# Kernel tuning notes

Measured on AMD Instinct MI355X. Metric: run time of the kernel, lower is better.

## Reference

```python
import jax, jax.numpy as jnp
import numpy as np

B, T, D, H = 4, 2048, 1024, 16
HD = D // H  # 64
LOCAL_CTX, BLOCKSIZE, VERTSIZE = 256, 1, 16
STRIDE = LOCAL_CTX // BLOCKSIZE  # 256


def build_fixed_mask(n):
    # num_verts == 1 branch of generate_fixed_attention_mask
    layout = np.zeros((n, n), dtype=np.bool_)
    # vertical stripes: top `vertsize` indices of each stride block
    for idx in range(STRIDE - VERTSIZE, STRIDE):
        layout[:, idx::STRIDE] = True
    rows = np.arange(n)
    # local: each query attends to its own stride-block
    same_block = (rows[:, None] // STRIDE) == (rows[None, :] // STRIDE)
    layout |= same_block
    # causal: zero out k > q
    layout &= rows[None, :] <= rows[:, None]
    return layout


def setup_inputs() -> dict:
    key = jax.random.key(0)
    k1, k2, k3, k4, k5 = jax.random.split(key, 5)
    s = 0.02
    return {
        "x": jax.random.normal(k1, (B, T, D), dtype=jnp.float32),
        "Wqkv": jax.random.normal(k2, (D, 3 * D), dtype=jnp.float32) * s,
        "bqkv": jax.random.normal(k3, (3 * D,), dtype=jnp.float32) * s,
        "Wproj": jax.random.normal(k4, (D, D), dtype=jnp.float32) * s,
        "bproj": jax.random.normal(k5, (D,), dtype=jnp.float32) * s,
        "mask": jnp.asarray(build_fixed_mask(T)),
    }


def reference(x, Wqkv, bqkv, Wproj, bproj, mask):
    b, t, _ = x.shape
    qkv = (x @ Wqkv + bqkv).reshape(b, t, 3, H, HD)
    # (B,T,3,H,HD) -> (B,H,T,HD) per component
    q = qkv[:, :, 0].transpose(0, 2, 1, 3)
    k = qkv[:, :, 1].transpose(0, 2, 1, 3)
    v = qkv[:, :, 2].transpose(0, 2, 1, 3)
    att = jnp.einsum("bhqd,bhkd->bhqk", q, k) * (1.0 / jnp.sqrt(jnp.float32(HD)))
    att = jnp.where(mask[:t, :t], att, -jnp.inf)
    att = jax.nn.softmax(att, axis=-1)
    y = jnp.einsum("bhqk,bhkd->bhqd", att, v)
    y = y.transpose(0, 2, 1, 3).reshape(b, t, D)
    return y @ Wproj + bproj
```

## Files before the change

kernel.cpp:

```cpp
#include <hip/hip_runtime.h>
#include <cstdint>
#include <cstddef>

typedef unsigned short u16;
typedef __attribute__((ext_vector_type(8))) short short8;
typedef __attribute__((ext_vector_type(4))) float f32x4;
typedef __attribute__((ext_vector_type(4))) unsigned short u16x4;

#define B_ 4
#define T_ 2048
#define D_ 1024
#define H_ 16
#define HD_ 64

__device__ __forceinline__ u16 f2bf(float f) {
  union { float f; unsigned i; } v; v.f = f;
  unsigned r = (v.i + 0x7FFFu + ((v.i >> 16) & 1u)) >> 16;
  return (u16)r;
}

__device__ __forceinline__ void load_lds16(const void* g, void* l) {
  __builtin_amdgcn_global_load_lds(
      (const __attribute__((address_space(1))) void*)g,
      (__attribute__((address_space(3))) void*)l, 16, 0, 0);
}

__global__ __launch_bounds__(256) void cvt_f32_bf16(const float* __restrict__ src,
                                                    u16* __restrict__ dst) {
  const size_t i = ((size_t)blockIdx.x * 256 + threadIdx.x) * 4;
  const f32x4 v = *(const f32x4*)(src + i);
  u16x4 o;
#pragma unroll
  for (int r = 0; r < 4; ++r) o[r] = f2bf(v[r]);
  *(u16x4*)(dst + i) = o;
}

__global__ __launch_bounds__(256) void transpose_cvt(const float* __restrict__ src,
                                                     u16* __restrict__ dst,
                                                     int R, int C) {
  __shared__ u16 t[32][33];
  const int c0 = blockIdx.x * 32, r0 = blockIdx.y * 32;
  const int tid = threadIdx.x;
  const int lr = tid >> 5, lc = tid & 31;
#pragma unroll
  for (int p = 0; p < 4; ++p)
    t[lr + p * 8][lc] = f2bf(src[(size_t)(r0 + lr + p * 8) * C + c0 + lc]);
  __syncthreads();
#pragma unroll
  for (int p = 0; p < 4; ++p)
    dst[(size_t)(c0 + lr + p * 8) * R + r0 + lc] = t[lc][lr + p * 8];
}

template <int EPI>
__global__ __launch_bounds__(256)
void gemm_bt(const u16* __restrict__ A, const u16* __restrict__ Bt,
             const float* __restrict__ bias, int K, int N,
             void* __restrict__ o0v, u16* __restrict__ o1, u16* __restrict__ o2) {
  __shared__ u16 As[128 * 32];
  __shared__ u16 Bs[128 * 32];
  const int tid = threadIdx.x;
  const int lane = tid & 63;
  const int w = tid >> 6;
  const int q = lane >> 4, col = lane & 15;
  const int m0 = blockIdx.y * 128, n0 = blockIdx.x * 128;
  const int wm = (w >> 1) * 64, wn = (w & 1) * 64;
  const int srow = tid >> 2;
  const int soff = (((tid & 3) ^ ((srow >> 1) & 3)) * 8);
  const int slot = (q ^ ((col >> 1) & 3)) * 8;

  f32x4 acc[4][4] = {};

  const u16* Ap = A + (size_t)(m0 + srow) * K + soff;
  const u16* Bp = Bt + (size_t)(n0 + srow) * K + soff;

  for (int kb = 0; kb < K; kb += 32) {
    load_lds16(Ap + kb, &As[tid * 8]);
    load_lds16(Ap + (size_t)64 * K + kb, &As[2048 + tid * 8]);
    load_lds16(Bp + kb, &Bs[tid * 8]);
    load_lds16(Bp + (size_t)64 * K + kb, &Bs[2048 + tid * 8]);
    __syncthreads();
    short8 af[4], bfr[4];
#pragma unroll
    for (int i = 0; i < 4; ++i)
      af[i] = *(const short8*)&As[(wm + i * 16 + col) * 32 + slot];
#pragma unroll
    for (int j = 0; j < 4; ++j)
      bfr[j] = *(const short8*)&Bs[(wn + j * 16 + col) * 32 + slot];
#pragma unroll
    for (int i = 0; i < 4; ++i)
#pragma unroll
      for (int j = 0; j < 4; ++j)
        acc[i][j] = __builtin_amdgcn_mfma_f32_16x16x32_bf16(af[i], bfr[j], acc[i][j], 0, 0, 0);
    __syncthreads();
  }

#pragma unroll
  for (int j = 0; j < 4; ++j) {
    const int n = n0 + wn + j * 16 + col;
    const float bv = bias[n];
    if constexpr (EPI == 0) {
      u16* q0p = (u16*)o0v;
      const int c = n >> 10, rem = n & 1023, hh = rem >> 6, dd = rem & 63;
#pragma unroll
      for (int i = 0; i < 4; ++i) {
        const int mrow = m0 + wm + i * 16 + q * 4;
        const int b = mrow >> 11, t = mrow & 2047;
        const int bh = b * H_ + hh;
        if (c == 0) {
#pragma unroll
          for (int r = 0; r < 4; ++r)
            q0p[((size_t)bh * T_ + t + r) * HD_ + dd] = f2bf((acc[i][j][r] + bv) * 0.125f);
        } else if (c == 1) {
#pragma unroll
          for (int r = 0; r < 4; ++r)
            o1[((size_t)bh * T_ + t + r) * HD_ + dd] = f2bf(acc[i][j][r] + bv);
        } else {
          u16x4 pk;
#pragma unroll
          for (int r = 0; r < 4; ++r) pk[r] = f2bf(acc[i][j][r] + bv);
          *(u16x4*)&o2[(size_t)bh * (T_ * HD_) + (size_t)(t >> 4) * (HD_ * 16) +
                       dd * 16 + (t & 15)] = pk;
        }
      }
    } else {
      float* outp = (float*)o0v;
#pragma unroll
      for (int i = 0; i < 4; ++i) {
        const int mrow = m0 + wm + i * 16 + q * 4;
#pragma unroll
        for (int r = 0; r < 4; ++r)
          outp[(size_t)(mrow + r) * N + n] = acc[i][j][r] + bv;
      }
    }
  }
}

__global__ __launch_bounds__(256)
void sparse_attn(const u16* __restrict__ Qb, const u16* __restrict__ Kb,
                 const u16* __restrict__ Vt, u16* __restrict__ Y) {
  const int tid = threadIdx.x, lane = tid & 63, wv = tid >> 6;
  const int cq = lane & 15, qd = lane >> 4;
  const int bh = blockIdx.y;
  const int qt = 31 - blockIdx.x;
  const int b = bh >> 4, hh = bh & 15;
  const int qb = qt >> 2;
  const int qg = qt * 64 + wv * 16;
  const u16* Qh = Qb + (size_t)bh * T_ * HD_;
  const u16* Kh = Kb + (size_t)bh * T_ * HD_;
  const u16* Vh = Vt + (size_t)bh * T_ * HD_;

  const short8 qf0 = *(const short8*)&Qh[(size_t)(qg + cq) * HD_ + qd * 8];
  const short8 qf1 = *(const short8*)&Qh[(size_t)(qg + cq) * HD_ + 32 + qd * 8];

  f32x4 o[4] = {};
  float lsum = 0.f;

  const int nloc = (qt & 3) * 4 + wv + 1;
  const int L = qb + nloc;

  for (int j = 0; j < L; ++j) {
    const int kb = (j < qb) ? (j * 256 + 240) : (qb * 256 + (j - qb) * 16);
    const bool diag = (j == L - 1);
    const short8 ka = *(const short8*)&Kh[(size_t)(kb + cq) * HD_ + qd * 8];
    const short8 kb8 = *(const short8*)&Kh[(size_t)(kb + cq) * HD_ + 32 + qd * 8];
    const u16* vblk = Vh + (size_t)(kb >> 4) * (HD_ * 16);
    short8 vf[4];
#pragma unroll
    for (int dt = 0; dt < 4; ++dt) {
      const u16x4 vv = *(const u16x4*)&vblk[(dt * 16 + cq) * 16 + qd * 4];
      vf[dt] = short8{(short)vv[0], (short)vv[1], (short)vv[2], (short)vv[3], 0, 0, 0, 0};
    }
    const f32x4 z = {0.f, 0.f, 0.f, 0.f};
    f32x4 s = __builtin_amdgcn_mfma_f32_16x16x32_bf16(ka, qf0, z, 0, 0, 0);
    s = __builtin_amdgcn_mfma_f32_16x16x32_bf16(kb8, qf1, s, 0, 0, 0);
    short8 p = {0, 0, 0, 0, 0, 0, 0, 0};
#pragma unroll
    for (int r = 0; r < 4; ++r) {
      float e = __expf(s[r]);
      if (diag && (qd * 4 + r) > cq) e = 0.f;
      lsum += e;
      p[r] = (short)f2bf(e);
    }
#pragma unroll
    for (int dt = 0; dt < 4; ++dt)
      o[dt] = __builtin_amdgcn_mfma_f32_16x16x32_bf16(vf[dt], p, o[dt], 0, 0, 0);
  }

  float lt = lsum + __shfl_xor(lsum, 16);
  lt += __shfl_xor(lt, 32);
  const float inv = 1.0f / lt;
#pragma unroll
  for (int dt = 0; dt < 4; ++dt) {
    u16x4 pk;
#pragma unroll
    for (int r = 0; r < 4; ++r) pk[r] = f2bf(o[dt][r] * inv);
    *(u16x4*)&Y[((size_t)(b * T_ + qg + cq)) * D_ + hh * HD_ + dt * 16 + qd * 4] = pk;
  }
}

extern "C" void kernel_launch(void* const* d_in, const int* in_sizes, int n_in,
                              void* d_out, int out_size, void* d_ws, size_t ws_size,
                              hipStream_t stream) {
  const float* x = (const float*)d_in[0];
  const float* Wqkv = (const float*)d_in[1];
  const float* bqkv = (const float*)d_in[2];
  const float* Wproj = (const float*)d_in[3];
  const float* bproj = (const float*)d_in[4];
  float* out = (float*)d_out;

  char* ws = (char*)d_ws;
  u16* xb     = (u16*)(ws + 0);
  u16* WqkvT  = (u16*)(ws + 16777216);
  u16* WprojT = (u16*)(ws + 23068672);
  u16* Qb     = (u16*)(ws + 25165824);
  u16* Kb     = (u16*)(ws + 41943040);
  u16* Vt     = (u16*)(ws + 58720256);
  u16* Y      = (u16*)(ws + 75497472);

  cvt_f32_bf16<<<dim3(8192), 256, 0, stream>>>(x, xb);
  transpose_cvt<<<dim3(96, 32), 256, 0, stream>>>(Wqkv, WqkvT, 1024, 3072);
  transpose_cvt<<<dim3(32, 32), 256, 0, stream>>>(Wproj, WprojT, 1024, 1024);
  gemm_bt<0><<<dim3(24, 64), 256, 0, stream>>>(xb, WqkvT, bqkv, 1024, 3072, Qb, Kb, Vt);
  sparse_attn<<<dim3(32, 64), 256, 0, stream>>>(Qb, Kb, Vt, Y);
  gemm_bt<1><<<dim3(8, 64), 256, 0, stream>>>(Y, WprojT, bproj, 1024, 1024, out, nullptr, nullptr);
}
```

Measured before the change: 286.1 us.

## Swap MFMA operands for row-contiguous epilogue stores and transpose V layout

Swaps the A/B operands of the GEMM MFMA so each lane holds four consecutive output columns. This lets the Q/K and projection epilogues write packed 4-wide vectors instead of scalar strided stores, and bias is loaded as a vector. V is now stored fully transposed ([bh][d][t]) rather than in 16-token tiles, so V stores in the epilogue become scalar writes strided by T while attention reads V from a T-strided layout. The change trades cheaper Q/K/output stores for less coalesced V writes.

```diff
diff --git a/kernel.cpp b/kernel.cpp
--- a/kernel.cpp
+++ b/kernel.cpp
@@ -52,10 +52,10 @@
 }
 
 template <int EPI>
-__global__ __launch_bounds__(256)
-void gemm_bt(const u16* __restrict__ A, const u16* __restrict__ Bt,
-             const float* __restrict__ bias, int K, int N,
-             void* __restrict__ o0v, u16* __restrict__ o1, u16* __restrict__ o2) {
+__device__ __forceinline__
+void gemm_body(const u16* __restrict__ A, const u16* __restrict__ Bt,
+               const float* __restrict__ bias, int K, int N,
+               void* __restrict__ o0v, u16* __restrict__ o1, u16* __restrict__ o2) {
   __shared__ u16 As[128 * 32];
   __shared__ u16 Bs[128 * 32];
   const int tid = threadIdx.x;
@@ -90,49 +90,84 @@
     for (int i = 0; i < 4; ++i)
 #pragma unroll
       for (int j = 0; j < 4; ++j)
-        acc[i][j] = __builtin_amdgcn_mfma_f32_16x16x32_bf16(af[i], bfr[j], acc[i][j], 0, 0, 0);
+        acc[i][j] = __builtin_amdgcn_mfma_f32_16x16x32_bf16(bfr[j], af[i], acc[i][j], 0, 0, 0);
     __syncthreads();
   }
 
-#pragma unroll
-  for (int j = 0; j < 4; ++j) {
-    const int n = n0 + wn + j * 16 + col;
-    const float bv = bias[n];
-    if constexpr (EPI == 0) {
-      u16* q0p = (u16*)o0v;
-      const int c = n >> 10, rem = n & 1023, hh = rem >> 6, dd = rem & 63;
+  f32x4 bv[4];
+#pragma unroll
+  for (int j = 0; j < 4; ++j)
+    bv[j] = *(const f32x4*)&bias[n0 + wn + j * 16 + q * 4];
+
+  if constexpr (EPI == 0) {
+    const int cuni = (n0 + wn) >> 10;
+    const int hh = ((n0 + wn) & 1023) >> 6;
+    const int b = (m0 + wm) >> 11;
+    const int bh = b * H_ + hh;
+    u16* q0p = (u16*)o0v;
+    if (cuni == 0) {
 #pragma unroll
       for (int i = 0; i < 4; ++i) {
-        const int mrow = m0 + wm + i * 16 + q * 4;
-        const int b = mrow >> 11, t = mrow & 2047;
-        const int bh = b * H_ + hh;
-        if (c == 0) {
+        const int t = (m0 + wm + i * 16 + col) & 2047;
+#pragma unroll
+        for (int j = 0; j < 4; ++j) {
+          u16x4 pk;
+#pragma unroll
+          for (int r = 0; r < 4; ++r) pk[r] = f2bf((acc[i][j][r] + bv[j][r]) * 0.125f);
+          *(u16x4*)&q0p[((size_t)bh * T_ + t) * HD_ + j * 16 + q * 4] = pk;
+        }
+      }
+    } else if (cuni == 1) {
+#pragma unroll
+      for (int i = 0; i < 4; ++i) {
+        const int t = (m0 + wm + i * 16 + col) & 2047;
+#pragma unroll
+        for (int j = 0; j < 4; ++j) {
+          u16x4 pk;
+#pragma unroll
+          for (int r = 0; r < 4; ++r) pk[r] = f2bf(acc[i][j][r] + bv[j][r]);
+          *(u16x4*)&o1[((size_t)bh * T_ + t) * HD_ + j * 16 + q * 4] = pk;
+        }
+      }
+    } else {
+#pragma unroll
+      for (int i = 0; i < 4; ++i) {
+        const int t = (m0 + wm + i * 16 + col) & 2047;
+#pragma unroll
+        for (int j = 0; j < 4; ++j)
 #pragma unroll
           for (int r = 0; r < 4; ++r)
-            q0p[((size_t)bh * T_ + t + r) * HD_ + dd] = f2bf((acc[i][j][r] + bv) * 0.125f);
-        } else if (c == 1) {
-#pragma unroll
-          for (int r = 0; r < 4; ++r)
-            o1[((size_t)bh * T_ + t + r) * HD_ + dd] = f2bf(acc[i][j][r] + bv);
-        } else {
-          u16x4 pk;
-#pragma unroll
-          for (int r = 0; r < 4; ++r) pk[r] = f2bf(acc[i][j][r] + bv);
-          *(u16x4*)&o2[(size_t)bh * (T_ * HD_) + (size_t)(t >> 4) * (HD_ * 16) +
-                       dd * 16 + (t & 15)] = pk;
-        }
-      }
-    } else {
-      float* outp = (float*)o0v;
-#pragma unroll
-      for (int i = 0; i < 4; ++i) {
-        const int mrow = m0 + wm + i * 16 + q * 4;
-#pragma unroll
-        for (int r = 0; r < 4; ++r)
-          outp[(size_t)(mrow + r) * N + n] = acc[i][j][r] + bv;
-      }
-    }
-  }
+            o2[((size_t)bh * HD_ + j * 16 + q * 4 + r) * T_ + t] =
+                f2bf(acc[i][j][r] + bv[j][r]);
+      }
+    }
+  } else {
+    float* outp = (float*)o0v;
+#pragma unroll
+    for (int i = 0; i < 4; ++i) {
+      const int m = m0 + wm + i * 16 + col;
+#pragma unroll
+      for (int j = 0; j < 4; ++j) {
+        f32x4 v;
+#pragma unroll
+        for (int r = 0; r < 4; ++r) v[r] = acc[i][j][r] + bv[j][r];
+        *(f32x4*)&outp[(size_t)m * N + n0 + wn + j * 16 + q * 4] = v;
+      }
+    }
+  }
+}
+
+__global__ __launch_bounds__(256)
+void gemm_qkv(const u16* __restrict__ A, const u16* __restrict__ Bt,
+              const float* __restrict__ bias, int K, int N,
+              void* __restrict__ o0v, u16* __restrict__ o1, u16* __restrict__ o2) {
+  gemm_body<0>(A, Bt, bias, K, N, o0v, o1, o2);
+}
+__global__ __launch_bounds__(256)
+void gemm_proj(const u16* __restrict__ A, const u16* __restrict__ Bt,
+               const float* __restrict__ bias, int K, int N,
+               void* __restrict__ o0v, u16* __restrict__ o1, u16* __restrict__ o2) {
+  gemm_body<1>(A, Bt, bias, K, N, o0v, o1, o2);
 }
 
 __global__ __launch_bounds__(256)
@@ -147,7 +182,7 @@
   const int qg = qt * 64 + wv * 16;
   const u16* Qh = Qb + (size_t)bh * T_ * HD_;
   const u16* Kh = Kb + (size_t)bh * T_ * HD_;
-  const u16* Vh = Vt + (size_t)bh * T_ * HD_;
+  const u16* Vh = Vt + (size_t)bh * HD_ * T_;
 
   const short8 qf0 = *(const short8*)&Qh[(size_t)(qg + cq) * HD_ + qd * 8];
   const short8 qf1 = *(const short8*)&Qh[(size_t)(qg + cq) * HD_ + 32 + qd * 8];
@@ -163,11 +198,10 @@
     const bool diag = (j == L - 1);
     const short8 ka = *(const short8*)&Kh[(size_t)(kb + cq) * HD_ + qd * 8];
     const short8 kb8 = *(const short8*)&Kh[(size_t)(kb + cq) * HD_ + 32 + qd * 8];
-    const u16* vblk = Vh + (size_t)(kb >> 4) * (HD_ * 16);
     short8 vf[4];
 #pragma unroll
     for (int dt = 0; dt < 4; ++dt) {
-      const u16x4 vv = *(const u16x4*)&vblk[(dt * 16 + cq) * 16 + qd * 4];
+      const u16x4 vv = *(const u16x4*)&Vh[(size_t)(dt * 16 + cq) * T_ + kb + qd * 4];
       vf[dt] = short8{(short)vv[0], (short)vv[1], (short)vv[2], (short)vv[3], 0, 0, 0, 0};
     }
     const f32x4 z = {0.f, 0.f, 0.f, 0.f};
@@ -220,7 +254,7 @@
   cvt_f32_bf16<<<dim3(8192), 256, 0, stream>>>(x, xb);
   transpose_cvt<<<dim3(96, 32), 256, 0, stream>>>(Wqkv, WqkvT, 1024, 3072);
   transpose_cvt<<<dim3(32, 32), 256, 0, stream>>>(Wproj, WprojT, 1024, 1024);
-  gemm_bt<0><<<dim3(24, 64), 256, 0, stream>>>(xb, WqkvT, bqkv, 1024, 3072, Qb, Kb, Vt);
+  gemm_qkv<<<dim3(24, 64), 256, 0, stream>>>(xb, WqkvT, bqkv, 1024, 3072, Qb, Kb, Vt);
   sparse_attn<<<dim3(32, 64), 256, 0, stream>>>(Qb, Kb, Vt, Y);
-  gemm_bt<1><<<dim3(8, 64), 256, 0, stream>>>(Y, WprojT, bproj, 1024, 1024, out, nullptr, nullptr);
-}
+  gemm_proj<<<dim3(8, 64), 256, 0, stream>>>(Y, WprojT, bproj, 1024, 1024, out, nullptr, nullptr);
+}
```

New measurement: 356.0 us. 1.24x slower.

## Split attention key blocks across waves with LDS reduction and prefetch

Applied to the files above, without the earlier changes.

Each block now handles one 16-query group, and its four waves split the key-block loop among themselves instead of each wave owning a different query group. Partial outputs and row sums are combined through LDS before normalisation. K/V loads are software-prefetched one iteration ahead, and V is stored as a plain transposed [d][T] layout. This targets load imbalance and serial latency in the per-wave loop, at the cost of an extra LDS reduction, a barrier and four times as many blocks.

```diff
diff --git a/kernel.cpp b/kernel.cpp
--- a/kernel.cpp
+++ b/kernel.cpp
@@ -52,10 +52,10 @@
 }
 
 template <int EPI>
-__global__ __launch_bounds__(256)
-void gemm_bt(const u16* __restrict__ A, const u16* __restrict__ Bt,
-             const float* __restrict__ bias, int K, int N,
-             void* __restrict__ o0v, u16* __restrict__ o1, u16* __restrict__ o2) {
+__device__ __forceinline__
+void gemm_body(const u16* __restrict__ A, const u16* __restrict__ Bt,
+               const float* __restrict__ bias, int K, int N,
+               void* __restrict__ o0v, u16* __restrict__ o1, u16* __restrict__ o2) {
   __shared__ u16 As[128 * 32];
   __shared__ u16 Bs[128 * 32];
   const int tid = threadIdx.x;
@@ -118,8 +118,7 @@
           u16x4 pk;
 #pragma unroll
           for (int r = 0; r < 4; ++r) pk[r] = f2bf(acc[i][j][r] + bv);
-          *(u16x4*)&o2[(size_t)bh * (T_ * HD_) + (size_t)(t >> 4) * (HD_ * 16) +
-                       dd * 16 + (t & 15)] = pk;
+          *(u16x4*)&o2[((size_t)bh * HD_ + dd) * T_ + t] = pk;
         }
       }
     } else {
@@ -136,18 +135,33 @@
 }
 
 __global__ __launch_bounds__(256)
+void gemm_qkv(const u16* __restrict__ A, const u16* __restrict__ Bt,
+              const float* __restrict__ bias, int K, int N,
+              void* __restrict__ o0v, u16* __restrict__ o1, u16* __restrict__ o2) {
+  gemm_body<0>(A, Bt, bias, K, N, o0v, o1, o2);
+}
+__global__ __launch_bounds__(256)
+void gemm_proj(const u16* __restrict__ A, const u16* __restrict__ Bt,
+               const float* __restrict__ bias, int K, int N,
+               void* __restrict__ o0v, u16* __restrict__ o1, u16* __restrict__ o2) {
+  gemm_body<1>(A, Bt, bias, K, N, o0v, o1, o2);
+}
+
+__global__ __launch_bounds__(256)
 void sparse_attn(const u16* __restrict__ Qb, const u16* __restrict__ Kb,
                  const u16* __restrict__ Vt, u16* __restrict__ Y) {
+  __shared__ float Osh[4][4][64][4];
+  __shared__ float Lsh[4][64];
   const int tid = threadIdx.x, lane = tid & 63, wv = tid >> 6;
   const int cq = lane & 15, qd = lane >> 4;
   const int bh = blockIdx.y;
-  const int qt = 31 - blockIdx.x;
+  const int G = 127 - (int)blockIdx.x;
   const int b = bh >> 4, hh = bh & 15;
-  const int qb = qt >> 2;
-  const int qg = qt * 64 + wv * 16;
+  const int qb = G >> 4;
+  const int qg = G * 16;
   const u16* Qh = Qb + (size_t)bh * T_ * HD_;
   const u16* Kh = Kb + (size_t)bh * T_ * HD_;
-  const u16* Vh = Vt + (size_t)bh * T_ * HD_;
+  const u16* Vh = Vt + (size_t)bh * HD_ * T_;
 
   const short8 qf0 = *(const short8*)&Qh[(size_t)(qg + cq) * HD_ + qd * 8];
   const short8 qf1 = *(const short8*)&Qh[(size_t)(qg + cq) * HD_ + 32 + qd * 8];
@@ -155,20 +169,31 @@
   f32x4 o[4] = {};
   float lsum = 0.f;
 
-  const int nloc = (qt & 3) * 4 + wv + 1;
-  const int L = qb + nloc;
-
-  for (int j = 0; j < L; ++j) {
+  const int L = qb + (G & 15) + 1;
+
+  short8 ka, kb8;
+  u16x4 vv[4];
+  int j = wv;
+  if (j < L) {
     const int kb = (j < qb) ? (j * 256 + 240) : (qb * 256 + (j - qb) * 16);
+    ka = *(const short8*)&Kh[(size_t)(kb + cq) * HD_ + qd * 8];
+    kb8 = *(const short8*)&Kh[(size_t)(kb + cq) * HD_ + 32 + qd * 8];
+#pragma unroll
+    for (int dt = 0; dt < 4; ++dt)
+      vv[dt] = *(const u16x4*)&Vh[(size_t)(dt * 16 + cq) * T_ + kb + qd * 4];
+  }
+  for (; j < L; j += 4) {
     const bool diag = (j == L - 1);
-    const short8 ka = *(const short8*)&Kh[(size_t)(kb + cq) * HD_ + qd * 8];
-    const short8 kb8 = *(const short8*)&Kh[(size_t)(kb + cq) * HD_ + 32 + qd * 8];
-    const u16* vblk = Vh + (size_t)(kb >> 4) * (HD_ * 16);
-    short8 vf[4];
-#pragma unroll
-    for (int dt = 0; dt < 4; ++dt) {
-      const u16x4 vv = *(const u16x4*)&vblk[(dt * 16 + cq) * 16 + qd * 4];
-      vf[dt] = short8{(short)vv[0], (short)vv[1], (short)vv[2], (short)vv[3], 0, 0, 0, 0};
+    short8 nka, nkb8;
+    u16x4 nvv[4];
+    const int jn = j + 4;
+    if (jn < L) {
+      const int kbn = (jn < qb) ? (jn * 256 + 240) : (qb * 256 + (jn - qb) * 16);
+      nka = *(const short8*)&Kh[(size_t)(kbn + cq) * HD_ + qd * 8];
+      nkb8 = *(const short8*)&Kh[(size_t)(kbn + cq) * HD_ + 32 + qd * 8];
+#pragma unroll
+      for (int dt = 0; dt < 4; ++dt)
+        nvv[dt] = *(const u16x4*)&Vh[(size_t)(dt * 16 + cq) * T_ + kbn + qd * 4];
     }
     const f32x4 z = {0.f, 0.f, 0.f, 0.f};
     f32x4 s = __builtin_amdgcn_mfma_f32_16x16x32_bf16(ka, qf0, z, 0, 0, 0);
@@ -182,20 +207,36 @@
       p[r] = (short)f2bf(e);
     }
 #pragma unroll
-    for (int dt = 0; dt < 4; ++dt)
-      o[dt] = __builtin_amdgcn_mfma_f32_16x16x32_bf16(vf[dt], p, o[dt], 0, 0, 0);
-  }
-
-  float lt = lsum + __shfl_xor(lsum, 16);
+    for (int dt = 0; dt < 4; ++dt) {
+      const short8 vf = {(short)vv[dt][0], (short)vv[dt][1], (short)vv[dt][2],
+                         (short)vv[dt][3], 0, 0, 0, 0};
+      o[dt] = __builtin_amdgcn_mfma_f32_16x16x32_bf16(vf, p, o[dt], 0, 0, 0);
+    }
+    ka = nka; kb8 = nkb8;
+#pragma unroll
+    for (int dt = 0; dt < 4; ++dt) vv[dt] = nvv[dt];
+  }
+
+#pragma unroll
+  for (int dt = 0; dt < 4; ++dt)
+    *(f32x4*)&Osh[wv][dt][lane][0] = o[dt];
+  Lsh[wv][lane] = lsum;
+  __syncthreads();
+
+  f32x4 acc = {0.f, 0.f, 0.f, 0.f};
+  float lt = 0.f;
+#pragma unroll
+  for (int w2 = 0; w2 < 4; ++w2) {
+    acc += *(const f32x4*)&Osh[w2][wv][lane][0];
+    lt += Lsh[w2][lane];
+  }
+  lt += __shfl_xor(lt, 16);
   lt += __shfl_xor(lt, 32);
   const float inv = 1.0f / lt;
-#pragma unroll
-  for (int dt = 0; dt < 4; ++dt) {
-    u16x4 pk;
-#pragma unroll
-    for (int r = 0; r < 4; ++r) pk[r] = f2bf(o[dt][r] * inv);
-    *(u16x4*)&Y[((size_t)(b * T_ + qg + cq)) * D_ + hh * HD_ + dt * 16 + qd * 4] = pk;
-  }
+  u16x4 pk;
+#pragma unroll
+  for (int r = 0; r < 4; ++r) pk[r] = f2bf(acc[r] * inv);
+  *(u16x4*)&Y[((size_t)(b * T_ + qg + cq)) * D_ + hh * HD_ + wv * 16 + qd * 4] = pk;
 }
 
 extern "C" void kernel_launch(void* const* d_in, const int* in_sizes, int n_in,
@@ -220,7 +261,7 @@
   cvt_f32_bf16<<<dim3(8192), 256, 0, stream>>>(x, xb);
   transpose_cvt<<<dim3(96, 32), 256, 0, stream>>>(Wqkv, WqkvT, 1024, 3072);
   transpose_cvt<<<dim3(32, 32), 256, 0, stream>>>(Wproj, WprojT, 1024, 1024);
-  gemm_bt<0><<<dim3(24, 64), 256, 0, stream>>>(xb, WqkvT, bqkv, 1024, 3072, Qb, Kb, Vt);
-  sparse_attn<<<dim3(32, 64), 256, 0, stream>>>(Qb, Kb, Vt, Y);
-  gemm_bt<1><<<dim3(8, 64), 256, 0, stream>>>(Y, WprojT, bproj, 1024, 1024, out, nullptr, nullptr);
-}
+  gemm_qkv<<<dim3(24, 64), 256, 0, stream>>>(xb, WqkvT, bqkv, 1024, 3072, Qb, Kb, Vt);
+  sparse_attn<<<dim3(128, 64), 256, 0, stream>>>(Qb, Kb, Vt, Y);
+  gemm_proj<<<dim3(8, 64), 256, 0, stream>>>(Y, WprojT, bproj, 1024, 1024, out, nullptr, nullptr);
+}
```

New measurement: 327.7 us. 14.6% more time.
